# Performance work log

Hardware: AMD Instinct MI355X
Metric: run time of the kernel (lower is better)

## Reference

```python
import jax, jax.numpy as jnp
import numpy as np

NUM_NODES = 100000
NUM_EDGES = 1600000
NUM_GRAPHS = 64
IN_CH, HID, NCLS = 15, 128, 11


def setup_inputs() -> dict:
    key = jax.random.key(0)
    ks = jax.random.split(key, 9)
    x = jax.random.normal(ks[0], (NUM_NODES, IN_CH), dtype=jnp.float32)
    edge_index = jax.random.randint(ks[1], (2, NUM_EDGES), 0, NUM_NODES, dtype=jnp.int64)
    batch = jnp.sort(jax.random.randint(ks[2], (NUM_NODES,), 0, NUM_GRAPHS, dtype=jnp.int64))
    s1 = 1.0 / np.sqrt(IN_CH)
    s2 = 1.0 / np.sqrt(HID)
    W1 = jax.random.normal(ks[3], (IN_CH, HID), dtype=jnp.float32) * s1
    b1 = jax.random.normal(ks[4], (HID,), dtype=jnp.float32) * s1
    W2 = jax.random.normal(ks[5], (HID, HID), dtype=jnp.float32) * s2
    b2 = jax.random.normal(ks[6], (HID,), dtype=jnp.float32) * s2
    Wf = jax.random.normal(ks[7], (HID, NCLS), dtype=jnp.float32) * s2
    bf = jax.random.normal(ks[8], (NCLS,), dtype=jnp.float32) * s2
    return {"x": x, "edge_index": edge_index, "batch": batch,
            "W1": W1, "b1": b1, "W2": W2, "b2": b2, "Wf": Wf, "bf": bf}


def reference(x, edge_index, batch, W1, b1, W2, b2, Wf, bf):
    N = x.shape[0]
    loop = jnp.arange(N, dtype=edge_index.dtype)
    # PyG GCNConv: add self-loops, symmetric D^{-1/2} A D^{-1/2} normalization
    src = jnp.concatenate([edge_index[0], loop])
    dst = jnp.concatenate([edge_index[1], loop])
    deg = jax.ops.segment_sum(jnp.ones(src.shape[0], dtype=x.dtype), dst, num_segments=N)
    dinv = deg ** -0.5  # deg >= 1 due to self-loops
    norm = (dinv[src] * dinv[dst])[:, None]  # [E+N, 1]

    def gcn(h, W, b):
        m = h @ W                                   # transform first (smaller gather)
        agg = jax.ops.segment_sum(m[src] * norm, dst, num_segments=N)
        return agg + b

    h = jax.nn.relu(gcn(x, W1, b1))
    h = jax.nn.relu(gcn(h, W2, b2))

    # global_mean_pool over graph ids
    sums = jax.ops.segment_sum(h, batch, num_segments=NUM_GRAPHS)
    cnts = jax.ops.segment_sum(jnp.ones((N,), dtype=h.dtype), batch, num_segments=NUM_GRAPHS)
    pooled = sums / jnp.maximum(cnts, 1.0)[:, None]  # [G, HID]
    return pooled @ Wf + bf                          # [G, NCLS]
```

## Files before the change

kernel.cpp:

```cpp
#include <hip/hip_runtime.h>

#define N_NODES 100000
#define N_EDGES 1600000
#define N_GRAPHS 64
#define IN_CH 15
#define HID 128
#define NCLS 11

#define NBUCK 196
#define NBF 512
#define EPB (N_EDGES / NBF)

using short8 = __attribute__((ext_vector_type(8))) short;
using f32x4 = __attribute__((ext_vector_type(4))) float;

__device__ __forceinline__ unsigned short f2bf(float f) {
    unsigned u = __builtin_bit_cast(unsigned, f);
    u += 0x7FFF + ((u >> 16) & 1);
    return (unsigned short)(u >> 16);
}
__device__ __forceinline__ unsigned packbf(float a, float b) {
    return (unsigned)f2bf(a) | ((unsigned)f2bf(b) << 16);
}
__device__ __forceinline__ float2 unpackbf(unsigned v) {
    float2 r;
    unsigned lo = v << 16;
    unsigned hi = v & 0xFFFF0000u;
    r.x = __builtin_bit_cast(float, lo);
    r.y = __builtin_bit_cast(float, hi);
    return r;
}

__global__ __launch_bounds__(256) void k_init(float* __restrict__ pooled) {
    int i = blockIdx.x * 256 + threadIdx.x;
    if (i < N_GRAPHS * HID) pooled[i] = 0.f;
}

__global__ __launch_bounds__(256) void k_hist(const int* __restrict__ dst,
                                              int* __restrict__ cntm) {
    __shared__ int hist[NBUCK];
    int t = threadIdx.x;
    for (int i = t; i < NBUCK; i += 256) hist[i] = 0;
    __syncthreads();
    int base = blockIdx.x * EPB;
#pragma unroll
    for (int i = 0; i < (EPB + 255) / 256; ++i) {
        int e = i * 256 + t;
        if (e < EPB) atomicAdd(&hist[dst[base + e] >> 9], 1);
    }
    __syncthreads();
    for (int b = t; b < NBUCK; b += 256)
        cntm[b * NBF + blockIdx.x] = hist[b];
}

__global__ __launch_bounds__(256) void k_btot(const int* __restrict__ cntm,
                                              int* __restrict__ tot) {
    __shared__ int red[256];
    int b = blockIdx.x, t = threadIdx.x;
    red[t] = cntm[b * NBF + t] + cntm[b * NBF + t + 256];
    __syncthreads();
    for (int off = 128; off > 0; off >>= 1) {
        if (t < off) red[t] += red[t + off];
        __syncthreads();
    }
    if (t == 0) tot[b] = red[0];
}

__global__ __launch_bounds__(256) void k_bscan(const int* __restrict__ tot,
                                               int* __restrict__ bbase,
                                               int* __restrict__ rowptr) {
    __shared__ int arr[256];
    int t = threadIdx.x;
    arr[t] = (t < NBUCK) ? tot[t] : 0;
    __syncthreads();
    for (int off = 1; off < 256; off <<= 1) {
        int v = (t >= off) ? arr[t - off] : 0;
        __syncthreads();
        arr[t] += v;
        __syncthreads();
    }
    if (t < NBUCK) bbase[t] = (t == 0) ? 0 : arr[t - 1];
    if (t == 0) rowptr[N_NODES] = N_EDGES;
}

__global__ __launch_bounds__(NBF) void k_offs(const int* __restrict__ cntm,
                                              const int* __restrict__ bbase,
                                              int* __restrict__ offs) {
    __shared__ int arr[NBF];
    int b = blockIdx.x, t = threadIdx.x;
    arr[t] = cntm[b * NBF + t];
    __syncthreads();
    for (int off = 1; off < NBF; off <<= 1) {
        int v = (t >= off) ? arr[t - off] : 0;
        __syncthreads();
        arr[t] += v;
        __syncthreads();
    }
    offs[b * NBF + t] = bbase[b] + ((t == 0) ? 0 : arr[t - 1]);
}

__global__ __launch_bounds__(256) void k_partition(const int* __restrict__ src,
                                                   const int* __restrict__ dst,
                                                   const int* __restrict__ offs,
                                                   unsigned* __restrict__ staging) {
    __shared__ int cur[NBUCK];
    int t = threadIdx.x;
    for (int b = t; b < NBUCK; b += 256) cur[b] = offs[b * NBF + blockIdx.x];
    __syncthreads();
    int base = blockIdx.x * EPB;
#pragma unroll
    for (int i = 0; i < (EPB + 255) / 256; ++i) {
        int e = i * 256 + t;
        if (e < EPB) {
            int d = dst[base + e];
            int s = src[base + e];
            int slot = atomicAdd(&cur[d >> 9], 1);
            staging[slot] = ((unsigned)(d & 511) << 17) | (unsigned)s;
        }
    }
}

__global__ __launch_bounds__(256) void k_fuse(const unsigned* __restrict__ staging,
                                              const int* __restrict__ bbase,
                                              int* __restrict__ rowptr,
                                              float* __restrict__ dinv,
                                              int* __restrict__ csr_src) {
    __shared__ int cnt[512];
    __shared__ int cur[512];
    __shared__ int arr[256];
    int b = blockIdx.x, t = threadIdx.x;
    cnt[t] = 0; cnt[t + 256] = 0;
    __syncthreads();
    int beg = bbase[b];
    int end = (b == NBUCK - 1) ? N_EDGES : bbase[b + 1];
    for (int e = beg + t; e < end; e += 256)
        atomicAdd(&cnt[staging[e] >> 17], 1);
    __syncthreads();
    int c0 = cnt[2 * t], c1 = cnt[2 * t + 1];
    arr[t] = c0 + c1;
    __syncthreads();
    for (int off = 1; off < 256; off <<= 1) {
        int v = (t >= off) ? arr[t - off] : 0;
        __syncthreads();
        arr[t] += v;
        __syncthreads();
    }
    int excl = (t == 0) ? 0 : arr[t - 1];
    int p0 = beg + excl;
    int p1 = p0 + c0;
    cur[2 * t] = p0;
    cur[2 * t + 1] = p1;
    int n0 = b << 9;
    int n = n0 + 2 * t;
    if (n < N_NODES) { rowptr[n] = p0; dinv[n] = rsqrtf((float)(c0 + 1)); }
    n = n0 + 2 * t + 1;
    if (n < N_NODES) { rowptr[n] = p1; dinv[n] = rsqrtf((float)(c1 + 1)); }
    __syncthreads();
    for (int e = beg + t; e < end; e += 256) {
        unsigned v = staging[e];
        int pos = atomicAdd(&cur[v >> 17], 1);
        csr_src[pos] = (int)(v & 0x1FFFFu);
    }
}

__global__ __launch_bounds__(256) void k_w2pack(const float* __restrict__ W2,
                                                uint4* __restrict__ Bp) {
    int i = blockIdx.x * 256 + threadIdx.x;
    if (i >= 2048) return;
    int lane = i & 63;
    int kb = (i >> 6) & 3;
    int ct = i >> 8;
    int col = ct * 16 + (lane & 15);
    int k0 = kb * 32 + ((lane >> 4) & 3) * 8;
    unsigned w[4];
#pragma unroll
    for (int p = 0; p < 4; ++p) {
        int k = k0 + 2 * p;
        w[p] = packbf(W2[k * HID + col], W2[(k + 1) * HID + col]);
    }
    Bp[i] = make_uint4(w[0], w[1], w[2], w[3]);
}

__global__ __launch_bounds__(256) void k_prescale(const float* __restrict__ x,
                                                  const float* __restrict__ dinv,
                                                  unsigned* __restrict__ xs) {
    int i = blockIdx.x * 256 + threadIdx.x;
    if (i >= N_NODES * 8) return;
    int n = i >> 3, p = i & 7;
    float dv = dinv[n];
    int c0 = 2 * p, c1 = c0 + 1;
    float a = x[(size_t)n * IN_CH + c0] * dv;
    float b = (c1 < IN_CH) ? x[(size_t)n * IN_CH + c1] * dv : 0.f;
    xs[i] = packbf(a, b);
}

__global__ __launch_bounds__(256) void k_gather15(const int* __restrict__ rowptr,
                                                  const int* __restrict__ csr_src,
                                                  const unsigned* __restrict__ xs,
                                                  const float* __restrict__ dinv,
                                                  float* __restrict__ agg) {
    int wave = (blockIdx.x * 256 + threadIdx.x) >> 6;
    if (wave >= N_NODES) return;
    int n = wave;
    int l = threadIdx.x & 63;
    int g = l >> 3, cp = l & 7;
    int beg = rowptr[n], end = rowptr[n + 1];
    float2 acc = make_float2(0.f, 0.f);
    for (int e = beg + g; e < end; e += 8) {
        int s = csr_src[e];
        float2 v = unpackbf(xs[(size_t)s * 8 + cp]);
        acc.x += v.x; acc.y += v.y;
    }
#pragma unroll
    for (int off = 8; off < 64; off <<= 1) {
        acc.x += __shfl_xor(acc.x, off, 64);
        acc.y += __shfl_xor(acc.y, off, 64);
    }
    if (l < 8) {
        float2 s = unpackbf(xs[(size_t)n * 8 + l]);
        float dv = dinv[n];
        float2 r = make_float2((acc.x + s.x) * dv, (acc.y + s.y) * dv);
        *(float2*)&agg[(size_t)n * 16 + 2 * l] = r;
    }
}

__global__ __launch_bounds__(256) void k_xform1b(const float* __restrict__ agg,
                                                 const float* __restrict__ W1,
                                                 const float* __restrict__ b1,
                                                 unsigned* __restrict__ h1b) {
    __shared__ float w[IN_CH * HID];
    int t = threadIdx.x;
    for (int i = t; i < IN_CH * HID; i += 256) w[i] = W1[i];
    __syncthreads();
    int node = blockIdx.x * 4 + (t >> 6);
    int lane = t & 63;
    int c = lane * 2;
    const float* ar = agg + (size_t)node * 16;
    float a0 = b1[c], a1 = b1[c + 1];
#pragma unroll
    for (int k = 0; k < IN_CH; ++k) {
        float av = ar[k];
        a0 += av * w[k * HID + c];
        a1 += av * w[k * HID + c + 1];
    }
    h1b[(size_t)node * 64 + lane] = packbf(fmaxf(a0, 0.f), fmaxf(a1, 0.f));
}

__global__ __launch_bounds__(256) void k_gather(const int* __restrict__ rowptr,
                                                const int* __restrict__ csr_src,
                                                const unsigned* __restrict__ m,
                                                const float* __restrict__ bias,
                                                const float* __restrict__ dinv,
                                                unsigned* __restrict__ outh) {
    int wave = (blockIdx.x * 256 + threadIdx.x) >> 6;
    if (wave >= N_NODES) return;
    int n = wave;
    int lane = threadIdx.x & 63;
    int c = lane * 2;
    int beg = rowptr[n], end = rowptr[n + 1];
    float2 acc = unpackbf(m[(size_t)n * 64 + lane]);
    int e = beg;
    for (; e + 8 <= end; e += 8) {
        int s0 = csr_src[e + 0], s1 = csr_src[e + 1], s2 = csr_src[e + 2], s3 = csr_src[e + 3];
        int s4 = csr_src[e + 4], s5 = csr_src[e + 5], s6 = csr_src[e + 6], s7 = csr_src[e + 7];
        unsigned v0 = m[(size_t)s0 * 64 + lane];
        unsigned v1 = m[(size_t)s1 * 64 + lane];
        unsigned v2 = m[(size_t)s2 * 64 + lane];
        unsigned v3 = m[(size_t)s3 * 64 + lane];
        unsigned v4 = m[(size_t)s4 * 64 + lane];
        unsigned v5 = m[(size_t)s5 * 64 + lane];
        unsigned v6 = m[(size_t)s6 * 64 + lane];
        unsigned v7 = m[(size_t)s7 * 64 + lane];
        float2 f0 = unpackbf(v0), f1 = unpackbf(v1), f2 = unpackbf(v2), f3 = unpackbf(v3);
        float2 f4 = unpackbf(v4), f5 = unpackbf(v5), f6 = unpackbf(v6), f7 = unpackbf(v7);
        acc.x += f0.x + f1.x + f2.x + f3.x + f4.x + f5.x + f6.x + f7.x;
        acc.y += f0.y + f1.y + f2.y + f3.y + f4.y + f5.y + f6.y + f7.y;
    }
    for (; e + 2 <= end; e += 2) {
        int s0 = csr_src[e], s1 = csr_src[e + 1];
        unsigned v0 = m[(size_t)s0 * 64 + lane];
        unsigned v1 = m[(size_t)s1 * 64 + lane];
        float2 f0 = unpackbf(v0), f1 = unpackbf(v1);
        acc.x += f0.x + f1.x;
        acc.y += f0.y + f1.y;
    }
    if (e < end) {
        float2 f = unpackbf(m[(size_t)csr_src[e] * 64 + lane]);
        acc.x += f.x; acc.y += f.y;
    }
    float dv = dinv[n];
    float2 b = *(const float2*)&bias[c];
    float rx = fmaxf(acc.x * dv + b.x, 0.f);
    float ry = fmaxf(acc.y * dv + b.y, 0.f);
    outh[(size_t)n * 64 + lane] = packbf(rx, ry);
}

__global__ __launch_bounds__(256) void k_xform2(const unsigned* __restrict__ h1b,
                                                const uint4* __restrict__ Bp,
                                                const float* __restrict__ dinv,
                                                unsigned short* __restrict__ mout) {
    int lane = threadIdx.x & 63;
    int wid = threadIdx.x >> 6;
    int row0 = blockIdx.x * 64 + wid * 16;
    int arow = row0 + (lane & 15);
    const uint4* hbase = (const uint4*)h1b;
    uint4 a_u[4];
#pragma unroll
    for (int kb = 0; kb < 4; ++kb)
        a_u[kb] = hbase[(size_t)arow * 16 + kb * 4 + (lane >> 4)];
    int rbase = row0 + (lane >> 4) * 4;
    float dv[4];
#pragma unroll
    for (int j = 0; j < 4; ++j) dv[j] = dinv[min(rbase + j, N_NODES - 1)];
#pragma unroll
    for (int ct = 0; ct < 8; ++ct) {
        f32x4 acc = {0.f, 0.f, 0.f, 0.f};
#pragma unroll
        for (int kb = 0; kb < 4; ++kb) {
            uint4 b_u = Bp[(ct * 4 + kb) * 64 + lane];
            acc = __builtin_amdgcn_mfma_f32_16x16x32_bf16(
                __builtin_bit_cast(short8, a_u[kb]),
                __builtin_bit_cast(short8, b_u), acc, 0, 0, 0);
        }
        int col = ct * 16 + (lane & 15);
#pragma unroll
        for (int j = 0; j < 4; ++j) {
            int r = rbase + j;
            if (r < N_NODES) mout[(size_t)r * HID + col] = f2bf(acc[j] * dv[j]);
        }
    }
}

__global__ __launch_bounds__(64) void k_cnt(const int* __restrict__ batch,
                                            int* __restrict__ cnt) {
    int g = threadIdx.x;
    if (g >= N_GRAPHS) return;
    int lo0 = 0, hi0 = N_NODES;
    while (lo0 < hi0) { int mid = (lo0 + hi0) >> 1; if (batch[mid] < g) lo0 = mid + 1; else hi0 = mid; }
    int lo1 = lo0, hi1 = N_NODES;
    while (lo1 < hi1) { int mid = (lo1 + hi1) >> 1; if (batch[mid] < g + 1) lo1 = mid + 1; else hi1 = mid; }
    cnt[g] = lo1 - lo0;
}

#define POOL_CHUNK 128
__global__ __launch_bounds__(256) void k_pool(const unsigned* __restrict__ h,
                                              const int* __restrict__ batch,
                                              float* __restrict__ pooled) {
    int t = threadIdx.x;
    int lane = t & 63;
    int grp = t >> 6;
    int start = blockIdx.x * POOL_CHUNK;
    int end = min(start + POOL_CHUNK, N_NODES);
    float2 acc = make_float2(0.f, 0.f);
    int cur = -1;
    for (int n = start + grp; n < end; n += 4) {
        int g = batch[n];
        if (g != cur) {
            if (cur >= 0) {
                atomicAdd(&pooled[cur * HID + lane * 2], acc.x);
                atomicAdd(&pooled[cur * HID + lane * 2 + 1], acc.y);
            }
            acc = make_float2(0.f, 0.f);
            cur = g;
        }
        float2 v = unpackbf(h[(size_t)n * 64 + lane]);
        acc.x += v.x; acc.y += v.y;
    }
    if (cur >= 0) {
        atomicAdd(&pooled[cur * HID + lane * 2], acc.x);
        atomicAdd(&pooled[cur * HID + lane * 2 + 1], acc.y);
    }
}

__global__ __launch_bounds__(128) void k_final(const float* __restrict__ pooled,
                                               const int* __restrict__ cnt,
                                               const float* __restrict__ Wf,
                                               const float* __restrict__ bf,
                                               float* __restrict__ out) {
    __shared__ float p[HID];
    int g = blockIdx.x, t = threadIdx.x;
    float inv = 1.f / fmaxf((float)cnt[g], 1.f);
    p[t] = pooled[g * HID + t] * inv;
    __syncthreads();
    if (t < NCLS) {
        float acc = bf[t];
        for (int k = 0; k < HID; ++k) acc += p[k] * Wf[k * NCLS + t];
        out[g * NCLS + t] = acc;
    }
}

extern "C" void kernel_launch(void* const* d_in, const int* in_sizes, int n_in,
                              void* d_out, int out_size, void* d_ws, size_t ws_size,
                              hipStream_t stream) {
    const float* x   = (const float*)d_in[0];
    const int*   ei  = (const int*)d_in[1];
    const int*   src = ei;
    const int*   dst = ei + N_EDGES;
    const int*   batch = (const int*)d_in[2];
    const float* W1 = (const float*)d_in[3];
    const float* b1 = (const float*)d_in[4];
    const float* W2 = (const float*)d_in[5];
    const float* b2 = (const float*)d_in[6];
    const float* Wf = (const float*)d_in[7];
    const float* bf = (const float*)d_in[8];
    float* out = (float*)d_out;

    char* ws = (char*)d_ws;
    size_t off = 0;
    unsigned* mbuf = (unsigned*)(ws + off);  off += (size_t)N_NODES * 64 * 4;
    unsigned* h1b = (unsigned*)(ws + off);   off += (size_t)N_NODES * 64 * 4;
    unsigned* h2b = (unsigned*)(ws + off);   off += (size_t)N_NODES * 64 * 4;
    int* csr_src = (int*)(ws + off);         off += (size_t)N_EDGES * 4;
    uint4* Bp = (uint4*)(ws + off);          off += (size_t)2048 * 16;
    float* dinv = (float*)(ws + off);        off += (size_t)N_NODES * 4;
    int* rowptr = (int*)(ws + off);          off += (size_t)(N_NODES + 1) * 4;
    int* cntm = (int*)(ws + off);            off += (size_t)NBUCK * NBF * 4;
    int* offs = (int*)(ws + off);            off += (size_t)NBUCK * NBF * 4;
    int* tot = (int*)(ws + off);             off += (size_t)NBUCK * 4;
    int* bbase = (int*)(ws + off);           off += (size_t)NBUCK * 4;
    float* pooled = (float*)(ws + off);      off += (size_t)N_GRAPHS * HID * 4;
    int* cnt = (int*)(ws + off);             off += (size_t)N_GRAPHS * 4;
    unsigned* staging = h2b;
    unsigned* xs = mbuf;
    float* agg = (float*)(mbuf + (size_t)N_NODES * 8);

    k_init<<<(N_GRAPHS * HID + 255) / 256, 256, 0, stream>>>(pooled);
    k_hist<<<NBF, 256, 0, stream>>>(dst, cntm);
    k_btot<<<NBUCK, 256, 0, stream>>>(cntm, tot);
    k_bscan<<<1, 256, 0, stream>>>(tot, bbase, rowptr);
    k_offs<<<NBUCK, NBF, 0, stream>>>(cntm, bbase, offs);
    k_partition<<<NBF, 256, 0, stream>>>(src, dst, offs, staging);
    k_fuse<<<NBUCK, 256, 0, stream>>>(staging, bbase, rowptr, dinv, csr_src);
    k_w2pack<<<8, 256, 0, stream>>>(W2, Bp);

    k_prescale<<<(N_NODES * 8 + 255) / 256, 256, 0, stream>>>(x, dinv, xs);
    k_gather15<<<(N_NODES + 3) / 4, 256, 0, stream>>>(rowptr, csr_src, xs, dinv, agg);
    k_xform1b<<<N_NODES / 4, 256, 0, stream>>>(agg, W1, b1, h1b);

    k_xform2<<<(N_NODES + 63) / 64, 256, 0, stream>>>(h1b, Bp, dinv, (unsigned short*)mbuf);
    k_gather<<<(N_NODES + 3) / 4, 256, 0, stream>>>(rowptr, csr_src, mbuf, b2, dinv, h2b);

    k_cnt<<<1, 64, 0, stream>>>(batch, cnt);
    k_pool<<<(N_NODES + POOL_CHUNK - 1) / POOL_CHUNK, 256, 0, stream>>>(h2b, batch, pooled);
    k_final<<<N_GRAPHS, 128, 0, stream>>>(pooled, cnt, Wf, bf, out);
}
```

Baseline: 248.0 us.

## Store layer-2 messages as column slices and gather per slice with edge-parallel lanes

k_xform2 now writes its bf16 output in eight 16-column slices, each laid out contiguously over all nodes, instead of row-major 128-wide rows. A new k_gather8 gives each block one slice. Each wave handles one node, with 8 lane groups each walking a different subset of edges and reading 32 bytes per neighbour, then combining the groups through shuffle reductions. The aim is a smaller per-slice working set that fits in cache during the random gather, plus more edge-level parallelism. The cost is eight times more blocks, re-reading csr_src once per slice, and extra shuffle work.

Result: slower. 452.1 us (+82.3%).

```diff
diff --git a/kernel.cpp b/kernel.cpp
--- a/kernel.cpp
+++ b/kernel.cpp
@@ -246,55 +246,6 @@
     h1b[(size_t)node * 64 + lane] = packbf(fmaxf(a0, 0.f), fmaxf(a1, 0.f));
 }
 
-__global__ __launch_bounds__(256) void k_gather(const int* __restrict__ rowptr,
-                                                const int* __restrict__ csr_src,
-                                                const unsigned* __restrict__ m,
-                                                const float* __restrict__ bias,
-                                                const float* __restrict__ dinv,
-                                                unsigned* __restrict__ outh) {
-    int wave = (blockIdx.x * 256 + threadIdx.x) >> 6;
-    if (wave >= N_NODES) return;
-    int n = wave;
-    int lane = threadIdx.x & 63;
-    int c = lane * 2;
-    int beg = rowptr[n], end = rowptr[n + 1];
-    float2 acc = unpackbf(m[(size_t)n * 64 + lane]);
-    int e = beg;
-    for (; e + 8 <= end; e += 8) {
-        int s0 = csr_src[e + 0], s1 = csr_src[e + 1], s2 = csr_src[e + 2], s3 = csr_src[e + 3];
-        int s4 = csr_src[e + 4], s5 = csr_src[e + 5], s6 = csr_src[e + 6], s7 = csr_src[e + 7];
-        unsigned v0 = m[(size_t)s0 * 64 + lane];
-        unsigned v1 = m[(size_t)s1 * 64 + lane];
-        unsigned v2 = m[(size_t)s2 * 64 + lane];
-        unsigned v3 = m[(size_t)s3 * 64 + lane];
-        unsigned v4 = m[(size_t)s4 * 64 + lane];
-        unsigned v5 = m[(size_t)s5 * 64 + lane];
-        unsigned v6 = m[(size_t)s6 * 64 + lane];
-        unsigned v7 = m[(size_t)s7 * 64 + lane];
-        float2 f0 = unpackbf(v0), f1 = unpackbf(v1), f2 = unpackbf(v2), f3 = unpackbf(v3);
-        float2 f4 = unpackbf(v4), f5 = unpackbf(v5), f6 = unpackbf(v6), f7 = unpackbf(v7);
-        acc.x += f0.x + f1.x + f2.x + f3.x + f4.x + f5.x + f6.x + f7.x;
-        acc.y += f0.y + f1.y + f2.y + f3.y + f4.y + f5.y + f6.y + f7.y;
-    }
-    for (; e + 2 <= end; e += 2) {
-        int s0 = csr_src[e], s1 = csr_src[e + 1];
-        unsigned v0 = m[(size_t)s0 * 64 + lane];
-        unsigned v1 = m[(size_t)s1 * 64 + lane];
-        float2 f0 = unpackbf(v0), f1 = unpackbf(v1);
-        acc.x += f0.x + f1.x;
-        acc.y += f0.y + f1.y;
-    }
-    if (e < end) {
-        float2 f = unpackbf(m[(size_t)csr_src[e] * 64 + lane]);
-        acc.x += f.x; acc.y += f.y;
-    }
-    float dv = dinv[n];
-    float2 b = *(const float2*)&bias[c];
-    float rx = fmaxf(acc.x * dv + b.x, 0.f);
-    float ry = fmaxf(acc.y * dv + b.y, 0.f);
-    outh[(size_t)n * 64 + lane] = packbf(rx, ry);
-}
-
 __global__ __launch_bounds__(256) void k_xform2(const unsigned* __restrict__ h1b,
                                                 const uint4* __restrict__ Bp,
                                                 const float* __restrict__ dinv,
@@ -312,6 +263,7 @@
     float dv[4];
 #pragma unroll
     for (int j = 0; j < 4; ++j) dv[j] = dinv[min(rbase + j, N_NODES - 1)];
+    int cloc = lane & 15;
 #pragma unroll
     for (int ct = 0; ct < 8; ++ct) {
         f32x4 acc = {0.f, 0.f, 0.f, 0.f};
@@ -322,12 +274,57 @@
                 __builtin_bit_cast(short8, a_u[kb]),
                 __builtin_bit_cast(short8, b_u), acc, 0, 0, 0);
         }
-        int col = ct * 16 + (lane & 15);
 #pragma unroll
         for (int j = 0; j < 4; ++j) {
             int r = rbase + j;
-            if (r < N_NODES) mout[(size_t)r * HID + col] = f2bf(acc[j] * dv[j]);
+            if (r < N_NODES)
+                mout[(size_t)ct * N_NODES * 16 + (size_t)r * 16 + cloc] = f2bf(acc[j] * dv[j]);
         }
+    }
+}
+
+__global__ __launch_bounds__(256) void k_gather8(const int* __restrict__ rowptr,
+                                                 const int* __restrict__ csr_src,
+                                                 const unsigned* __restrict__ ms,
+                                                 const float* __restrict__ bias,
+                                                 const float* __restrict__ dinv,
+                                                 unsigned* __restrict__ outh) {
+    int slice = blockIdx.x & 7;
+    int node = (blockIdx.x >> 3) * 4 + (threadIdx.x >> 6);
+    if (node >= N_NODES) return;
+    int l = threadIdx.x & 63;
+    int g = l >> 3, cp = l & 7;
+    const unsigned* m = ms + (size_t)slice * N_NODES * 8;
+    int beg = rowptr[node], end = rowptr[node + 1];
+    float2 acc = make_float2(0.f, 0.f);
+    int e = beg + g;
+    for (; e + 8 < end; e += 16) {
+        int s0 = __builtin_nontemporal_load(&csr_src[e]);
+        int s1 = __builtin_nontemporal_load(&csr_src[e + 8]);
+        unsigned v0 = m[(size_t)s0 * 8 + cp];
+        unsigned v1 = m[(size_t)s1 * 8 + cp];
+        float2 f0 = unpackbf(v0), f1 = unpackbf(v1);
+        acc.x += f0.x + f1.x;
+        acc.y += f0.y + f1.y;
+    }
+    if (e < end) {
+        int s = __builtin_nontemporal_load(&csr_src[e]);
+        float2 f = unpackbf(m[(size_t)s * 8 + cp]);
+        acc.x += f.x; acc.y += f.y;
+    }
+#pragma unroll
+    for (int off = 8; off < 64; off <<= 1) {
+        acc.x += __shfl_xor(acc.x, off, 64);
+        acc.y += __shfl_xor(acc.y, off, 64);
+    }
+    if (l < 8) {
+        float2 s = unpackbf(m[(size_t)node * 8 + l]);
+        float dv = dinv[node];
+        int c = slice * 16 + 2 * l;
+        float2 b = *(const float2*)&bias[c];
+        float rx = fmaxf((acc.x + s.x) * dv + b.x, 0.f);
+        float ry = fmaxf((acc.y + s.y) * dv + b.y, 0.f);
+        outh[(size_t)node * 64 + slice * 8 + l] = packbf(rx, ry);
     }
 }
 
@@ -438,7 +435,7 @@
     k_xform1b<<<N_NODES / 4, 256, 0, stream>>>(agg, W1, b1, h1b);
 
     k_xform2<<<(N_NODES + 63) / 64, 256, 0, stream>>>(h1b, Bp, dinv, (unsigned short*)mbuf);
-    k_gather<<<(N_NODES + 3) / 4, 256, 0, stream>>>(rowptr, csr_src, mbuf, b2, dinv, h2b);
+    k_gather8<<<((N_NODES + 3) / 4) * 8, 256, 0, stream>>>(rowptr, csr_src, mbuf, b2, dinv, h2b);
 
     k_cnt<<<1, 64, 0, stream>>>(batch, cnt);
     k_pool<<<(N_NODES + POOL_CHUNK - 1) / POOL_CHUNK, 256, 0, stream>>>(h2b, batch, pooled);
```
